# Optimization experiments

Measured on AMD Instinct MI355X. Metric: run time of the kernel, lower is better.

## Reference

```python
import jax, jax.numpy as jnp
import numpy as np

EPS = 1e-5

def headwise_linear(x, w):
    # x: [B,S,D], w: [NH, DH_out, DH_in] block-diagonal linear per head
    B, S, D = x.shape
    NH, O, DH = w.shape
    xh = x.reshape(B, S, NH, DH)
    return jnp.einsum('bshd,hod->bsho', xh, w).reshape(B, S, NH * O)

def setup_inputs() -> dict:
    key = jax.random.key(0)
    ks = jax.random.split(key, 10)
    B, S, D, NH, K = 8, 4096, 768, 4, 4
    DH = D // NH
    small = (2.0 / (5.0 * D)) ** 0.5  # small_init scale
    return {
        'x': jax.random.normal(ks[0], (B, S, D), jnp.float32),
        'conv_w': jax.random.normal(ks[1], (D, 1, K), jnp.float32) * (1.0 / K ** 0.5),
        'conv_b': jnp.zeros((D,), jnp.float32),
        'w_f': jax.random.normal(ks[2], (NH, DH, DH), jnp.float32) * small,
        'w_i': jax.random.normal(ks[3], (NH, DH, DH), jnp.float32) * small,
        'w_z': jax.random.normal(ks[4], (NH, DH, DH), jnp.float32) * small,
        'w_o': jax.random.normal(ks[5], (NH, DH, DH), jnp.float32) * small,
        'r_kernel': jax.random.normal(ks[6], (NH, DH, 4, DH), jnp.float32) * (1.0 / DH ** 0.5),
        'r_bias': jnp.zeros((4, NH, DH), jnp.float32),
        'gn_weight': jnp.ones((D,), jnp.float32),
    }

def reference(x, conv_w, conv_b, w_f, w_i, w_z, w_o, r_kernel, r_bias, gn_weight):
    B, S, D = x.shape
    NH, DH = r_kernel.shape[0], r_kernel.shape[1]
    K = conv_w.shape[-1]
    # --- causal depthwise conv1d + SiLU ---
    xt = jnp.transpose(x, (0, 2, 1))  # [B,D,S]
    xc = jax.lax.conv_general_dilated(xt, conv_w, (1,), [(K - 1, 0)],
                                      feature_group_count=D)
    x_conv = jax.nn.silu(jnp.transpose(xc + conv_b[None, :, None], (0, 2, 1)))
    # --- headwise gate projections (note: original code feeds fgate->i, igate->f) ---
    gi = headwise_linear(x_conv, w_f)
    gf = headwise_linear(x_conv, w_i)
    gz = headwise_linear(x, w_z)
    go = headwise_linear(x, w_o)
    Wx = jnp.stack([gi, gf, gz, go], axis=2).reshape(B, S, 4, NH, DH)
    Wx = jnp.transpose(Wx, (1, 0, 2, 3, 4))  # [S,B,4,NH,DH]
    # --- sLSTM recurrent scan with exponential gating + stabilizer m ---
    def step(carry, wx_t):
        y, c, n, m = carry  # each [B,NH,DH]
        Ry = jnp.einsum('bhd,hdge->bghe', y, r_kernel)  # [B,4,NH,DH]
        raw = wx_t + Ry + r_bias[None]
        iraw, fraw, zraw, oraw = raw[:, 0], raw[:, 1], raw[:, 2], raw[:, 3]
        logfplusm = m + jax.nn.log_sigmoid(fraw)
        mnew = jnp.maximum(iraw, logfplusm)
        igate = jnp.exp(iraw - mnew)
        fgate = jnp.exp(logfplusm - mnew)
        cnew = fgate * c + igate * jnp.tanh(zraw)
        nnew = fgate * n + igate
        ynew = jax.nn.sigmoid(oraw) * cnew / nnew
        return (ynew, cnew, nnew, mnew), ynew
    init = tuple(jnp.zeros((B, NH, DH), x.dtype) for _ in range(4))
    _, ys = jax.lax.scan(step, init, Wx)  # [S,B,NH,DH]
    y = jnp.transpose(ys, (1, 2, 0, 3))  # [B,NH,S,DH]
    # --- multi-head layer norm (group norm with NH groups over DH) ---
    mean = y.mean(-1, keepdims=True)
    var = y.var(-1, keepdims=True)
    yn = (y - mean) * jax.lax.rsqrt(var + EPS)
    yn = yn * gn_weight.reshape(1, NH, 1, DH)
    return jnp.transpose(yn, (0, 2, 1, 3)).reshape(B, S, NH * DH)
```

## Files before the change

### kernel.cpp

```cpp
#include <hip/hip_runtime.h>
#include <hip/hip_bf16.h>
#include <math.h>

#define B_ 8
#define S_ 4096
#define D_ 768
#define NH_ 4
#define DH_ 192
#define G_ 4
#define NTOT_ 768

typedef __attribute__((ext_vector_type(8))) short short8;
typedef __attribute__((ext_vector_type(4))) float floatx4;

__device__ __forceinline__ short f2bs(float f) {
  union { float f; unsigned u; } v; v.f = f;
  unsigned r = v.u + 0x7FFFu + ((v.u >> 16) & 1u);
  return (short)(r >> 16);
}
__device__ __forceinline__ float bs2f(unsigned short s) {
  union { unsigned u; float f; } v; v.u = ((unsigned)s) << 16;
  return v.f;
}

__global__ __launch_bounds__(256) void wconv_kernel(
    const float* __restrict__ wf, const float* __restrict__ wi,
    const float* __restrict__ wz, const float* __restrict__ wo,
    short* __restrict__ Wbf)
{
  int idx = blockIdx.x * 256 + threadIdx.x;
  int hg = idx / (DH_ * DH_);
  int r  = idx % (DH_ * DH_);
  int h = hg >> 2, g = hg & 3;
  const float* W = (g == 0) ? wf : (g == 1) ? wi : (g == 2) ? wz : wo;
  Wbf[idx] = f2bs(W[(size_t)h * DH_ * DH_ + r]);
}

__global__ __launch_bounds__(256) void conv_silu_kernel(
    const float* __restrict__ x, const float* __restrict__ cw, const float* __restrict__ cb,
    short* __restrict__ xb, short* __restrict__ xcb)
{
  const int b  = blockIdx.x / (S_ / 64);
  const int s0 = (blockIdx.x % (S_ / 64)) * 64;
  const int tid = threadIdx.x;
  float wv[3][4], bias[3], win[3][3];
  for (int j = 0; j < 3; ++j) {
    int d = tid + j * 256;
    for (int k = 0; k < 4; ++k) wv[j][k] = cw[d * 4 + k];
    bias[j] = cb[d];
    for (int p = 0; p < 3; ++p) {
      int s = s0 - 3 + p;
      win[j][p] = (s >= 0) ? x[((size_t)b * S_ + s) * D_ + d] : 0.f;
    }
  }
  for (int i = 0; i < 64; ++i) {
    size_t base = ((size_t)b * S_ + (s0 + i)) * D_;
    for (int j = 0; j < 3; ++j) {
      int d = tid + j * 256;
      float xc = x[base + d];
      float a = bias[j] + win[j][0] * wv[j][0] + win[j][1] * wv[j][1]
                        + win[j][2] * wv[j][2] + xc * wv[j][3];
      float sv = a / (1.f + __expf(-a));
      xb[base + d]  = f2bs(xc);
      xcb[base + d] = f2bs(sv);
      win[j][0] = win[j][1]; win[j][1] = win[j][2]; win[j][2] = xc;
    }
  }
}

__global__ __launch_bounds__(256) void proj_kernel(
    const short* __restrict__ xb, const short* __restrict__ xcb,
    const short* __restrict__ Wbf, short* __restrict__ P)
{
  const int hg = blockIdx.y;
  const int h = hg >> 2, g = hg & 3;
  const short* A  = (g < 2) ? xcb : xb;
  const short* Wb = Wbf + (size_t)hg * (DH_ * DH_);
  const int tid = threadIdx.x, w = tid >> 6, l = tid & 63;
  const int l15 = l & 15, lg = l >> 4;
  const int R0 = blockIdx.x * 256 + w * 64;

  for (int mp = 0; mp < 2; ++mp) {
    const int rb0 = R0 + mp * 32;
    floatx4 acc[2][12];
    for (int u = 0; u < 2; ++u)
      for (int nt = 0; nt < 12; ++nt) acc[u][nt] = (floatx4){0.f, 0.f, 0.f, 0.f};
    const short* Ar = A + (size_t)(rb0 + l15) * D_ + h * DH_ + lg * 8;
    const short* Bp = Wb + l15 * DH_ + lg * 8;
    for (int kk = 0; kk < 6; ++kk) {
      short8 a0 = *(const short8*)(Ar + kk * 32);
      short8 a1 = *(const short8*)(Ar + (size_t)16 * D_ + kk * 32);
      for (int nt = 0; nt < 12; ++nt) {
        short8 bf = *(const short8*)(Bp + nt * 16 * DH_ + kk * 32);
        acc[0][nt] = __builtin_amdgcn_mfma_f32_16x16x32_bf16(a0, bf, acc[0][nt], 0, 0, 0);
        acc[1][nt] = __builtin_amdgcn_mfma_f32_16x16x32_bf16(a1, bf, acc[1][nt], 0, 0, 0);
      }
    }
    for (int u = 0; u < 2; ++u) {
      for (int q = 0; q < 4; ++q) {
        int row = rb0 + u * 16 + lg * 4 + q;
        int s = row & (S_ - 1);
        int bb = row >> 12;
        size_t ob = ((size_t)(s * NH_ + h) * B_ + bb) * NTOT_ + g * DH_ + l15;
        for (int nt = 0; nt < 12; ++nt) P[ob + nt * 16] = f2bs(acc[u][nt][q]);
      }
    }
  }
}

__global__ __launch_bounds__(512, 2) void scan_kernel(
    const short* __restrict__ P, const float* __restrict__ rk,
    const float* __restrict__ rb, const float* __restrict__ gnw,
    float* __restrict__ out)
{
  const int bid = blockIdx.x;
  const int b = bid >> 2, h = bid & 3;
  const int tid = threadIdx.x;
  const int w = tid >> 6, l = tid & 63;
  const int l15 = l & 15, lg = l >> 4;

  __shared__ short y_lds[DH_];
  __shared__ float raw_lds[NTOT_];
  __shared__ float stats_lds[8];

  short8 Bf[6][6];
  {
    const float* Rm = rk + (size_t)h * DH_ * NTOT_;
    for (int i = 0; i < 6; ++i) {
      int n = (w * 6 + i) * 16 + l15;
      for (int kk = 0; kk < 6; ++kk) {
        int kb = kk * 32 + lg * 8;
        short8 v;
        for (int j = 0; j < 8; ++j) v[j] = f2bs(Rm[(size_t)(kb + j) * NTOT_ + n]);
        Bf[i][kk] = v;
      }
    }
  }

  float biasv[4] = {0.f, 0.f, 0.f, 0.f};
  float gw = 0.f;
  if (tid < DH_) {
    for (int g = 0; g < 4; ++g) biasv[g] = rb[(g * NH_ + h) * DH_ + tid];
    gw = gnw[h * DH_ + tid];
    y_lds[tid] = 0;
  }

  float c = 0.f, nrm = 0.f, m = 0.f, yprev = 0.f;
  const short* Pb = P + ((size_t)h * B_ + b) * NTOT_;
  float wxc[4] = {0.f, 0.f, 0.f, 0.f};
  if (tid < DH_) {
    for (int g = 0; g < 4; ++g) wxc[g] = bs2f((unsigned short)Pb[g * DH_ + tid]);
  }
  unsigned short wxn[4] = {0, 0, 0, 0};
  __syncthreads();

  for (int t = 0; t < S_; ++t) {
    if (tid < DH_ && t + 1 < S_) {
      const short* Pt = Pb + (size_t)(t + 1) * (NH_ * B_ * NTOT_);
      for (int g = 0; g < 4; ++g) wxn[g] = (unsigned short)Pt[g * DH_ + tid];
    }
    if (t > 0 && tid < DH_) {
      float s0 = stats_lds[0] + stats_lds[2] + stats_lds[4];
      float s1 = stats_lds[1] + stats_lds[3] + stats_lds[5];
      float mean = s0 * (1.f / DH_);
      float var = s1 * (1.f / DH_) - mean * mean;
      float rs = rsqrtf(var + 1e-5f);
      out[((size_t)b * S_ + (t - 1)) * D_ + h * DH_ + tid] = (yprev - mean) * rs * gw;
    }
    short8 Af[6];
    for (int kk = 0; kk < 6; ++kk)
      Af[kk] = *(const short8*)&y_lds[kk * 32 + lg * 8];
    floatx4 acc[6];
    for (int i = 0; i < 6; ++i) acc[i] = (floatx4){0.f, 0.f, 0.f, 0.f};
    for (int kk = 0; kk < 6; ++kk)
      for (int i = 0; i < 6; ++i)
        acc[i] = __builtin_amdgcn_mfma_f32_16x16x32_bf16(Af[kk], Bf[i][kk], acc[i], 0, 0, 0);
    if (l < 16) {
      for (int i = 0; i < 6; ++i) raw_lds[(w * 6 + i) * 16 + l] = acc[i][0];
    }
    __syncthreads();
    if (tid < DH_) {
      float ir  = wxc[0] + raw_lds[tid] + biasv[0];
      float fr  = wxc[1] + raw_lds[DH_ + tid] + biasv[1];
      float zr  = wxc[2] + raw_lds[2 * DH_ + tid] + biasv[2];
      float orr = wxc[3] + raw_lds[3 * DH_ + tid] + biasv[3];
      float lsf = (fr >= 0.f) ? (0.f - log1pf(__expf(-fr))) : (fr - log1pf(__expf(fr)));
      float lfm = m + lsf;
      float mnew = fmaxf(ir, lfm);
      float ig = __expf(ir - mnew);
      float fg = __expf(lfm - mnew);
      float e2z = __expf(2.f * zr);
      float tz = 1.f - 2.f / (e2z + 1.f);
      c   = fg * c + ig * tz;
      nrm = fg * nrm + ig;
      m = mnew;
      float sg = 1.f / (1.f + __expf(-orr));
      float y = sg * c / nrm;
      yprev = y;
      y_lds[tid] = f2bs(y);
      float ps = y, pq = y * y;
      for (int off = 32; off >= 1; off >>= 1) {
        ps += __shfl_xor(ps, off);
        pq += __shfl_xor(pq, off);
      }
      if (l == 0) { stats_lds[w * 2] = ps; stats_lds[w * 2 + 1] = pq; }
      for (int g = 0; g < 4; ++g) wxc[g] = bs2f(wxn[g]);
    }
    __syncthreads();
  }
  if (tid < DH_) {
    float s0 = stats_lds[0] + stats_lds[2] + stats_lds[4];
    float s1 = stats_lds[1] + stats_lds[3] + stats_lds[5];
    float mean = s0 * (1.f / DH_);
    float var = s1 * (1.f / DH_) - mean * mean;
    float rs = rsqrtf(var + 1e-5f);
    out[((size_t)b * S_ + (S_ - 1)) * D_ + h * DH_ + tid] = (yprev - mean) * rs * gw;
  }
}

extern "C" void kernel_launch(void* const* d_in, const int* in_sizes, int n_in,
                              void* d_out, int out_size, void* d_ws, size_t ws_size,
                              hipStream_t stream) {
  const float* x   = (const float*)d_in[0];
  const float* cw  = (const float*)d_in[1];
  const float* cb  = (const float*)d_in[2];
  const float* wf  = (const float*)d_in[3];
  const float* wi  = (const float*)d_in[4];
  const float* wz  = (const float*)d_in[5];
  const float* wo  = (const float*)d_in[6];
  const float* rk  = (const float*)d_in[7];
  const float* rb  = (const float*)d_in[8];
  const float* gnw = (const float*)d_in[9];
  float* out = (float*)d_out;

  short* P   = (short*)d_ws;
  short* Wbf = (short*)((char*)d_ws + (size_t)201326592);
  short* xb  = (short*)d_out;
  short* xcb = (short*)((char*)d_out + (size_t)50331648);

  wconv_kernel<<<dim3(2304), 256, 0, stream>>>(wf, wi, wz, wo, Wbf);
  conv_silu_kernel<<<dim3(512), 256, 0, stream>>>(x, cw, cb, xb, xcb);
  proj_kernel<<<dim3(128, 16), 256, 0, stream>>>(xb, xcb, Wbf, P);
  scan_kernel<<<dim3(32), 512, 0, stream>>>(P, rk, rb, gnw, out);
}
```

Measured before the change: 5.979 ms.

## Rewrite sLSTM scan with per-thread fp16 dot2 recurrence and separate groupnorm kernel

The scan now assigns one thread per (element, gate) pair across 768 threads. Each thread keeps its column of the recurrent matrix in registers as fp16 pairs and computes the recurrent product with fdot2 instead of MFMA plus an LDS round trip. Gate values are exchanged among groups of four lanes with DPP broadcasts, and y is double-buffered in LDS so each step needs only one barrier. Group norm moves to a separate parallel kernel that reads fp16 y written back into P, whose layout becomes per-(head,batch) contiguous. The trade-off is lower precision (fp16 recurrent weights and y) and extra global traffic for the y round trip.

```diff
diff --git a/kernel.cpp b/kernel.cpp
--- a/kernel.cpp
+++ b/kernel.cpp
@@ -7,11 +7,12 @@
 #define D_ 768
 #define NH_ 4
 #define DH_ 192
-#define G_ 4
 #define NTOT_ 768
 
 typedef __attribute__((ext_vector_type(8))) short short8;
 typedef __attribute__((ext_vector_type(4))) float floatx4;
+typedef _Float16 f16;
+typedef __attribute__((ext_vector_type(2))) _Float16 h2;
 
 __device__ __forceinline__ short f2bs(float f) {
   union { float f; unsigned u; } v; v.f = f;
@@ -21,6 +22,21 @@
 __device__ __forceinline__ float bs2f(unsigned short s) {
   union { unsigned u; float f; } v; v.u = ((unsigned)s) << 16;
   return v.f;
+}
+
+#if __has_builtin(__builtin_amdgcn_fdot2)
+__device__ __forceinline__ float FDOT2(h2 a, h2 b, float c) {
+  return __builtin_amdgcn_fdot2(a, b, c, false);
+}
+#else
+__device__ __forceinline__ float FDOT2(h2 a, h2 b, float c) {
+  return c + (float)a.x * (float)b.x + (float)a.y * (float)b.y;
+}
+#endif
+
+template<int CTRL>
+__device__ __forceinline__ float qbcast(float x) {
+  return __int_as_float(__builtin_amdgcn_mov_dpp(__float_as_int(x), CTRL, 0xf, 0xf, true));
 }
 
 __global__ __launch_bounds__(256) void wconv_kernel(
@@ -101,121 +117,122 @@
         int row = rb0 + u * 16 + lg * 4 + q;
         int s = row & (S_ - 1);
         int bb = row >> 12;
-        size_t ob = ((size_t)(s * NH_ + h) * B_ + bb) * NTOT_ + g * DH_ + l15;
+        size_t ob = (((size_t)h * B_ + bb) * S_ + s) * NTOT_ + g * DH_ + l15;
         for (int nt = 0; nt < 12; ++nt) P[ob + nt * 16] = f2bs(acc[u][nt][q]);
       }
     }
   }
 }
 
-__global__ __launch_bounds__(512, 2) void scan_kernel(
-    const short* __restrict__ P, const float* __restrict__ rk,
-    const float* __restrict__ rb, const float* __restrict__ gnw,
+__global__ __launch_bounds__(768) void scan_kernel(
+    short* P_, const float* __restrict__ rk, const float* __restrict__ rb)
+{
+  const int bid = blockIdx.x;
+  const int h = bid >> 3;
+  const int t0 = threadIdx.x;
+  const int e = t0 >> 2, g = t0 & 3;
+
+  __shared__ __align__(16) f16 y_lds[2][DH_];
+
+  h2 Rr[96];
+  {
+    const float* Rc = rk + (size_t)h * (DH_ * NTOT_) + g * DH_ + e;
+#pragma unroll
+    for (int j = 0; j < 96; ++j) {
+      float v0 = Rc[(size_t)(2 * j) * NTOT_];
+      float v1 = Rc[(size_t)(2 * j + 1) * NTOT_];
+      Rr[j] = (h2){(f16)v0, (f16)v1};
+    }
+  }
+  const float biasv = rb[(g * NH_ + h) * DH_ + e];
+  if (t0 < DH_) y_lds[0][t0] = (f16)0.f;
+
+  float c = 0.f, nrm = 0.f, m = 0.f;
+  short* Pc = P_ + (size_t)bid * S_ * NTOT_;
+  const int addr = g * DH_ + e;
+  float wxc = bs2f((unsigned short)Pc[addr]);
+  __syncthreads();
+
+#pragma unroll 1
+  for (int t = 0; t < S_; ++t) {
+    unsigned short wxn = 0;
+    if (t + 1 < S_) wxn = (unsigned short)Pc[(size_t)(t + 1) * NTOT_ + addr];
+
+    const int cur = t & 1, nxt = cur ^ 1;
+    const f16* yb = &y_lds[cur][0];
+    float a0 = 0.f, a1 = 0.f, a2 = 0.f, a3 = 0.f;
+#pragma unroll
+    for (int j = 0; j < 96; j += 4) {
+      h2 y0 = *(const h2*)(yb + 2 * j);
+      h2 y1 = *(const h2*)(yb + 2 * j + 2);
+      h2 y2 = *(const h2*)(yb + 2 * j + 4);
+      h2 y3 = *(const h2*)(yb + 2 * j + 6);
+      a0 = FDOT2(Rr[j],     y0, a0);
+      a1 = FDOT2(Rr[j + 1], y1, a1);
+      a2 = FDOT2(Rr[j + 2], y2, a2);
+      a3 = FDOT2(Rr[j + 3], y3, a3);
+    }
+    float raw = wxc + ((a0 + a1) + (a2 + a3)) + biasv;
+
+    float ir  = qbcast<0x00>(raw);
+    float fr  = qbcast<0x55>(raw);
+    float zr  = qbcast<0xAA>(raw);
+    float orr = qbcast<0xFF>(raw);
+
+    float lsf = fminf(fr, 0.f) - __logf(1.f + __expf(-fabsf(fr)));
+    float lfm = m + lsf;
+    float mnew = fmaxf(ir, lfm);
+    float ig = __expf(ir - mnew);
+    float fg = __expf(lfm - mnew);
+    float e2z = __expf(2.f * zr);
+    float tz = 1.f - 2.f / (e2z + 1.f);
+    c   = fg * c + ig * tz;
+    nrm = fg * nrm + ig;
+    m = mnew;
+    float sg = 1.f / (1.f + __expf(-orr));
+    float y = sg * c / nrm;
+
+    f16 yh = (f16)y;
+    if (g == 0) {
+      y_lds[nxt][e] = yh;
+      union { f16 h; short s; } uv; uv.h = yh;
+      Pc[(size_t)t * NTOT_ + e] = uv.s;
+    }
+    wxc = bs2f(wxn);
+    __syncthreads();
+  }
+}
+
+__global__ __launch_bounds__(256) void gnorm_kernel(
+    const short* __restrict__ yws, const float* __restrict__ gnw,
     float* __restrict__ out)
 {
-  const int bid = blockIdx.x;
-  const int b = bid >> 2, h = bid & 3;
-  const int tid = threadIdx.x;
-  const int w = tid >> 6, l = tid & 63;
-  const int l15 = l & 15, lg = l >> 4;
-
-  __shared__ short y_lds[DH_];
-  __shared__ float raw_lds[NTOT_];
-  __shared__ float stats_lds[8];
-
-  short8 Bf[6][6];
-  {
-    const float* Rm = rk + (size_t)h * DH_ * NTOT_;
-    for (int i = 0; i < 6; ++i) {
-      int n = (w * 6 + i) * 16 + l15;
-      for (int kk = 0; kk < 6; ++kk) {
-        int kb = kk * 32 + lg * 8;
-        short8 v;
-        for (int j = 0; j < 8; ++j) v[j] = f2bs(Rm[(size_t)(kb + j) * NTOT_ + n]);
-        Bf[i][kk] = v;
-      }
-    }
-  }
-
-  float biasv[4] = {0.f, 0.f, 0.f, 0.f};
-  float gw = 0.f;
-  if (tid < DH_) {
-    for (int g = 0; g < 4; ++g) biasv[g] = rb[(g * NH_ + h) * DH_ + tid];
-    gw = gnw[h * DH_ + tid];
-    y_lds[tid] = 0;
-  }
-
-  float c = 0.f, nrm = 0.f, m = 0.f, yprev = 0.f;
-  const short* Pb = P + ((size_t)h * B_ + b) * NTOT_;
-  float wxc[4] = {0.f, 0.f, 0.f, 0.f};
-  if (tid < DH_) {
-    for (int g = 0; g < 4; ++g) wxc[g] = bs2f((unsigned short)Pb[g * DH_ + tid]);
-  }
-  unsigned short wxn[4] = {0, 0, 0, 0};
-  __syncthreads();
-
-  for (int t = 0; t < S_; ++t) {
-    if (tid < DH_ && t + 1 < S_) {
-      const short* Pt = Pb + (size_t)(t + 1) * (NH_ * B_ * NTOT_);
-      for (int g = 0; g < 4; ++g) wxn[g] = (unsigned short)Pt[g * DH_ + tid];
-    }
-    if (t > 0 && tid < DH_) {
-      float s0 = stats_lds[0] + stats_lds[2] + stats_lds[4];
-      float s1 = stats_lds[1] + stats_lds[3] + stats_lds[5];
-      float mean = s0 * (1.f / DH_);
-      float var = s1 * (1.f / DH_) - mean * mean;
-      float rs = rsqrtf(var + 1e-5f);
-      out[((size_t)b * S_ + (t - 1)) * D_ + h * DH_ + tid] = (yprev - mean) * rs * gw;
-    }
-    short8 Af[6];
-    for (int kk = 0; kk < 6; ++kk)
-      Af[kk] = *(const short8*)&y_lds[kk * 32 + lg * 8];
-    floatx4 acc[6];
-    for (int i = 0; i < 6; ++i) acc[i] = (floatx4){0.f, 0.f, 0.f, 0.f};
-    for (int kk = 0; kk < 6; ++kk)
-      for (int i = 0; i < 6; ++i)
-        acc[i] = __builtin_amdgcn_mfma_f32_16x16x32_bf16(Af[kk], Bf[i][kk], acc[i], 0, 0, 0);
-    if (l < 16) {
-      for (int i = 0; i < 6; ++i) raw_lds[(w * 6 + i) * 16 + l] = acc[i][0];
-    }
-    __syncthreads();
-    if (tid < DH_) {
-      float ir  = wxc[0] + raw_lds[tid] + biasv[0];
-      float fr  = wxc[1] + raw_lds[DH_ + tid] + biasv[1];
-      float zr  = wxc[2] + raw_lds[2 * DH_ + tid] + biasv[2];
-      float orr = wxc[3] + raw_lds[3 * DH_ + tid] + biasv[3];
-      float lsf = (fr >= 0.f) ? (0.f - log1pf(__expf(-fr))) : (fr - log1pf(__expf(fr)));
-      float lfm = m + lsf;
-      float mnew = fmaxf(ir, lfm);
-      float ig = __expf(ir - mnew);
-      float fg = __expf(lfm - mnew);
-      float e2z = __expf(2.f * zr);
-      float tz = 1.f - 2.f / (e2z + 1.f);
-      c   = fg * c + ig * tz;
-      nrm = fg * nrm + ig;
-      m = mnew;
-      float sg = 1.f / (1.f + __expf(-orr));
-      float y = sg * c / nrm;
-      yprev = y;
-      y_lds[tid] = f2bs(y);
-      float ps = y, pq = y * y;
-      for (int off = 32; off >= 1; off >>= 1) {
-        ps += __shfl_xor(ps, off);
-        pq += __shfl_xor(pq, off);
-      }
-      if (l == 0) { stats_lds[w * 2] = ps; stats_lds[w * 2 + 1] = pq; }
-      for (int g = 0; g < 4; ++g) wxc[g] = bs2f(wxn[g]);
-    }
-    __syncthreads();
-  }
-  if (tid < DH_) {
-    float s0 = stats_lds[0] + stats_lds[2] + stats_lds[4];
-    float s1 = stats_lds[1] + stats_lds[3] + stats_lds[5];
-    float mean = s0 * (1.f / DH_);
-    float var = s1 * (1.f / DH_) - mean * mean;
-    float rs = rsqrtf(var + 1e-5f);
-    out[((size_t)b * S_ + (S_ - 1)) * D_ + h * DH_ + tid] = (yprev - mean) * rs * gw;
-  }
+  const int row = blockIdx.x * 4 + (threadIdx.x >> 6);
+  const int l = threadIdx.x & 63;
+  const int h = row >> 15;
+  const int b = (row >> 12) & 7;
+  const int s = row & (S_ - 1);
+  const short* yr = yws + (size_t)row * NTOT_;
+  float v[3];
+  float su = 0.f, sq = 0.f;
+#pragma unroll
+  for (int j = 0; j < 3; ++j) {
+    unsigned short u = (unsigned short)yr[l + j * 64];
+    union { unsigned short u; f16 h; } cv; cv.u = u;
+    v[j] = (float)cv.h;
+    su += v[j]; sq += v[j] * v[j];
+  }
+  for (int off = 32; off; off >>= 1) {
+    su += __shfl_xor(su, off);
+    sq += __shfl_xor(sq, off);
+  }
+  float mean = su * (1.f / DH_);
+  float var = sq * (1.f / DH_) - mean * mean;
+  float rs = rsqrtf(var + 1e-5f);
+  float* orow = out + ((size_t)b * S_ + s) * D_ + h * DH_;
+#pragma unroll
+  for (int j = 0; j < 3; ++j)
+    orow[l + j * 64] = (v[j] - mean) * rs * gnw[h * DH_ + l + j * 64];
 }
 
 extern "C" void kernel_launch(void* const* d_in, const int* in_sizes, int n_in,
@@ -241,5 +258,6 @@
   wconv_kernel<<<dim3(2304), 256, 0, stream>>>(wf, wi, wz, wo, Wbf);
   conv_silu_kernel<<<dim3(512), 256, 0, stream>>>(x, cw, cb, xb, xcb);
   proj_kernel<<<dim3(128, 16), 256, 0, stream>>>(xb, xcb, Wbf, P);
-  scan_kernel<<<dim3(32), 512, 0, stream>>>(P, rk, rb, gnw, out);
-}
+  scan_kernel<<<dim3(32), 768, 0, stream>>>(P, rk, rb);
+  gnorm_kernel<<<dim3(32768), 256, 0, stream>>>(P, gnw, out);
+}
```

After: 5.831 ms. -2.5%, faster.
